# Performance work log

Measured on AMD Instinct MI355X. Metric: run time of the kernel, lower is better.

## Reference

```python
import jax, jax.numpy as jnp
import numpy as np

N_NODES = 50000
N_EDGES = 1000000
N_QUERY = 100000
NUM_FEATURES = 256
HIDDEN = 256
LABEL_DIM = 2


def glorot(key, shape):
    lim = float(np.sqrt(6.0 / (shape[0] + shape[1])))
    return jax.random.uniform(key, shape, jnp.float32, -lim, lim)


def setup_inputs() -> dict:
    key = jax.random.key(0)
    ks = jax.random.split(key, 8)
    x = jax.random.normal(ks[0], (N_NODES, NUM_FEATURES), jnp.float32)
    edge_index = jax.random.randint(ks[1], (2, N_EDGES), 0, N_NODES)
    query_edges = jax.random.randint(ks[2], (N_QUERY, 2), 0, N_NODES)
    edge_weight = jax.random.uniform(ks[3], (N_EDGES,), jnp.float32)
    W1 = glorot(ks[4], (NUM_FEATURES, HIDDEN))
    b1 = jnp.zeros((HIDDEN,), jnp.float32)
    W2 = glorot(ks[5], (HIDDEN, HIDDEN))
    b2 = jnp.zeros((HIDDEN,), jnp.float32)
    Wl = glorot(ks[6], (2 * HIDDEN, LABEL_DIM))
    bl = jnp.zeros((LABEL_DIM,), jnp.float32)
    return {"x": x, "edge_index": edge_index, "query_edges": query_edges,
            "edge_weight": edge_weight, "W1": W1, "b1": b1, "W2": W2,
            "b2": b2, "Wl": Wl, "bl": bl}


def digcn_conv(x, edge_index, edge_weight, W, b):
    # x: [N, F_in] -> h: [N, F_out]; propagate: out[dst] += w_e * h[src]
    h = x @ W
    src, dst = edge_index[0], edge_index[1]
    msg = h[src] * edge_weight[:, None]            # [E, F_out]
    agg = jax.ops.segment_sum(msg, dst, num_segments=x.shape[0])
    return agg + b


def reference(x, edge_index, query_edges, edge_weight, W1, b1, W2, b2, Wl, bl):
    h = jax.nn.relu(digcn_conv(x, edge_index, edge_weight, W1, b1))
    # dropout is identity at eval time
    h = digcn_conv(h, edge_index, edge_weight, W2, b2)
    q = jnp.concatenate((h[query_edges[:, 0]], h[query_edges[:, 1]]), axis=-1)
    logits = q @ Wl + bl
    return jax.nn.log_softmax(logits, axis=1)
```

## Files before the change

### kernel.cpp

```cpp
#include <hip/hip_runtime.h>
#include <hip/hip_bf16.h>
#include <math.h>

typedef __bf16 bf16;
typedef __bf16 v8bf __attribute__((ext_vector_type(8)));
typedef __bf16 v4bf __attribute__((ext_vector_type(4)));
typedef float  v4f  __attribute__((ext_vector_type(4)));

#define FDIM 256
#define BKT_CAP 8192
#define AROW 264
#define GEMM_BLOCKS 352
#define K3_BLOCKS 512
#define P3_BLOCKS (K3_BLOCKS - GEMM_BLOCKS)


__global__ __launch_bounds__(256) void flag_kernel(float* __restrict__ out, int n) {
  int i = blockIdx.x * 256 + threadIdx.x;
  if (i < n) out[i] = 1.0e9f;
}

__global__ __launch_bounds__(256) void k1_prep(const float* __restrict__ W1,
                                               const float* __restrict__ W2,
                                               bf16* __restrict__ Wt1,
                                               const int* __restrict__ dst,
                                               int* __restrict__ phist,
                                               const float* __restrict__ Wl,
                                               const float* __restrict__ b2,
                                               const float* __restrict__ bl,
                                               float4* __restrict__ V,
                                               float* __restrict__ cc,
                                               int E, int N, int nbkt) {
  __shared__ int h[256];
  __shared__ float sWl[1024];
  __shared__ float red[256];
  int b = blockIdx.x;
  int t = threadIdx.x;
  if (b < 256) {
    int k = b;
    Wt1[t * FDIM + k] = (bf16)W1[k * FDIM + t];
  } else if (b < 512) {
    int pb = b - 256;
    h[t] = 0;
    __syncthreads();
    for (int e = pb * 256 + t; e < E; e += 256 * 256) {
      int d = dst[e];
      d = d < 0 ? 0 : (d >= N ? N - 1 : d);
      atomicAdd(&h[d >> 8], 1);
    }
    __syncthreads();
    phist[pb * 256 + t] = h[t];
  } else {
#pragma unroll
    for (int j = 0; j < 4; ++j) sWl[j * 256 + t] = Wl[j * 256 + t];
    __syncthreads();
    const float* w2row = W2 + (size_t)t * FDIM;
    float4 acc = make_float4(0.f, 0.f, 0.f, 0.f);
    for (int j = 0; j < 256; ++j) {
      float w = w2row[j];
      acc.x += w * sWl[2 * j + 0];
      acc.y += w * sWl[2 * j + 1];
      acc.z += w * sWl[512 + 2 * j + 0];
      acc.w += w * sWl[512 + 2 * j + 1];
    }
    V[t] = acc;
    float bj = b2[t];
    red[t] = bj * (sWl[2 * t + 0] + sWl[512 + 2 * t + 0]);
    __syncthreads();
    if (t == 0) {
      float s = 0.f;
      for (int j = 0; j < 256; ++j) s += red[j];
      cc[0] = s + bl[0];
    }
    __syncthreads();
    red[t] = bj * (sWl[2 * t + 1] + sWl[512 + 2 * t + 1]);
    __syncthreads();
    if (t == 0) {
      float s = 0.f;
      for (int j = 0; j < 256; ++j) s += red[j];
      cc[1] = s + bl[1];
    }
  }
}

__global__ __launch_bounds__(256) void p2_scan(const int* __restrict__ phist,
                                               int* __restrict__ bbase,
                                               int* __restrict__ gcur,
                                               int* __restrict__ offs,
                                               int nbkt, int Nn) {
  __shared__ int wsum[4];
  int t = threadIdx.x, lane = t & 63, wv = t >> 6;
  int v = 0;
  for (int pb = 0; pb < 256; ++pb) v += phist[pb * 256 + t];
  if (t >= nbkt) v = 0;
  int x = v;
#pragma unroll
  for (int d = 1; d < 64; d <<= 1) {
    int y = __shfl_up(x, d, 64);
    if (lane >= d) x += y;
  }
  if (lane == 63) wsum[wv] = x;
  __syncthreads();
  int woff = 0;
  if (wv >= 1) woff += wsum[0];
  if (wv >= 2) woff += wsum[1];
  if (wv >= 3) woff += wsum[2];
  int incl = woff + x;
  int excl = incl - v;
  if (t < nbkt) { bbase[t] = excl; gcur[t] = excl; }
  if (t == 255) {
    bbase[nbkt] = incl;
    offs[Nn] = incl;
  }
}


__device__ inline void stage64(const float* __restrict__ A, bf16* __restrict__ As,
                               int row0, int M, int tid) {
#pragma unroll
  for (int j = 0; j < 8; ++j) {
    int g = j * 2048 + tid * 8;
    int r = g >> 8, c = g & 255;
    int gr = row0 + r; if (gr >= M) gr = M - 1;
    const float* p = A + (size_t)gr * FDIM + c;
    float4 f0 = *reinterpret_cast<const float4*>(p);
    float4 f1 = *reinterpret_cast<const float4*>(p + 4);
    v8bf o;
    o[0] = (bf16)f0.x; o[1] = (bf16)f0.y; o[2] = (bf16)f0.z; o[3] = (bf16)f0.w;
    o[4] = (bf16)f1.x; o[5] = (bf16)f1.y; o[6] = (bf16)f1.z; o[7] = (bf16)f1.w;
    *reinterpret_cast<v8bf*>(As + r * AROW + c) = o;
  }
}

__device__ inline void gemm_body(const float* __restrict__ A, const bf16* __restrict__ Bt,
                                 bf16* __restrict__ C, int M, int bid, int nblocks,
                                 bf16* __restrict__ As) {
  const int K = FDIM, N = FDIM;
  int tid = threadIdx.x;
  int wave = tid >> 6;
  int lane = tid & 63;
  int l15 = lane & 15, quad = lane >> 4;

  v8bf bfr[4][8];
#pragma unroll
  for (int nn = 0; nn < 4; ++nn) {
    const bf16* bp = Bt + (size_t)(wave * 64 + nn * 16 + l15) * K + quad * 8;
#pragma unroll
    for (int kk = 0; kk < 8; ++kk)
      bfr[nn][kk] = *reinterpret_cast<const v8bf*>(bp + kk * 32);
  }

  int ntiles = (M + 63) >> 6;
  for (int tile = bid; tile < ntiles; tile += nblocks) {
    int row0 = tile * 64;
    __syncthreads();
    stage64(A, As, row0, M, tid);
    __syncthreads();

#pragma unroll
    for (int st = 0; st < 4; ++st) {
      v8bf afr[8];
#pragma unroll
      for (int kk = 0; kk < 8; ++kk)
        afr[kk] = *reinterpret_cast<const v8bf*>(As + (st * 16 + l15) * AROW + quad * 8 + kk * 32);

      v4f acc[4];
#pragma unroll
      for (int nn = 0; nn < 4; ++nn) acc[nn] = (v4f){0.f, 0.f, 0.f, 0.f};

#pragma unroll
      for (int kk = 0; kk < 8; ++kk)
#pragma unroll
        for (int nn = 0; nn < 4; ++nn)
          acc[nn] = __builtin_amdgcn_mfma_f32_16x16x32_bf16(afr[kk], bfr[nn][kk], acc[nn], 0, 0, 0);

#pragma unroll
      for (int nn = 0; nn < 4; ++nn)
#pragma unroll
        for (int r = 0; r < 4; ++r) {
          int row = row0 + st * 16 + quad * 4 + r;
          int col = wave * 64 + nn * 16 + l15;
          if (row < M) C[(size_t)row * N + col] = (bf16)acc[nn][r];
        }
    }
  }
}

__device__ inline void p3_body(const int* __restrict__ src, const int* __restrict__ dst,
                               const float* __restrict__ ew, int* __restrict__ gcur,
                               uint2* __restrict__ tmp, int E, int N, int nbkt,
                               int pb, int nblocks, int* h, int* base, int* cnt) {
  int t = threadIdx.x;
  int chunk = (E + nblocks - 1) / nblocks;
  int lo = pb * chunk;
  int hi = lo + chunk; if (hi > E) hi = E;
  h[t] = 0; cnt[t] = 0;
  __syncthreads();
  for (int e = lo + t; e < hi; e += 256) {
    int d = dst[e];
    d = d < 0 ? 0 : (d >= N ? N - 1 : d);
    atomicAdd(&h[d >> 8], 1);
  }
  __syncthreads();
  if (t < nbkt) base[t] = atomicAdd(&gcur[t], h[t]);
  __syncthreads();
  for (int e = lo + t; e < hi; e += 256) {
    int d = dst[e];
    d = d < 0 ? 0 : (d >= N ? N - 1 : d);
    int b = d >> 8;
    int sv = src[e];
    sv = sv < 0 ? 0 : (sv >= N ? N - 1 : sv);
    unsigned int u = __float_as_uint(ew[e]);
    unsigned int wbits = ((u + 0x7FFFu + ((u >> 16) & 1u)) & 0xFFFF0000u);
    unsigned int meta = wbits | (unsigned int)(sv & 0xFFFF);
    int r = atomicAdd(&cnt[b], 1);
    int pos = base[b] + r;
    if (pos >= 0 && pos < E) tmp[pos] = make_uint2(meta, (unsigned int)d);
  }
}

__global__ __launch_bounds__(256, 2) void k3_gemm1_p3(const float* __restrict__ x,
                                                      const bf16* __restrict__ Wt1,
                                                      bf16* __restrict__ bufT, int M,
                                                      const int* __restrict__ src,
                                                      const int* __restrict__ dst,
                                                      const float* __restrict__ ew,
                                                      int* __restrict__ gcur,
                                                      uint2* __restrict__ tmp,
                                                      int E, int N, int nbkt) {
  __shared__ bf16 As[64 * AROW];
  __shared__ int h[256], base[256], cnt[256];
  if (blockIdx.x < GEMM_BLOCKS)
    gemm_body(x, Wt1, bufT, M, blockIdx.x, GEMM_BLOCKS, As);
  else
    p3_body(src, dst, ew, gcur, tmp, E, N, nbkt, blockIdx.x - GEMM_BLOCKS, P3_BLOCKS,
            h, base, cnt);
}

__global__ __launch_bounds__(256) void p4_sort(const uint2* __restrict__ tmp,
                                               const int* __restrict__ bbase,
                                               unsigned int* __restrict__ pmeta,
                                               int* __restrict__ offs,
                                               int Nn, int E) {
  __shared__ uint2 ent[BKT_CAP];
  __shared__ int h2[256], ex2[256], c2[256];
  __shared__ int wsum[4];
  int b = blockIdx.x, t = threadIdx.x, lane = t & 63, wv = t >> 6;
  int s0 = bbase[b], s1 = bbase[b + 1];
  int count = s1 - s0;
  if (count < 0) count = 0;
  if (count > BKT_CAP) count = BKT_CAP;
  for (int i = t; i < count; i += 256) ent[i] = tmp[s0 + i];
  h2[t] = 0; c2[t] = 0;
  __syncthreads();
  for (int i = t; i < count; i += 256) atomicAdd(&h2[ent[i].y & 255u], 1);
  __syncthreads();
  int v = h2[t];
  int x = v;
#pragma unroll
  for (int d = 1; d < 64; d <<= 1) {
    int y = __shfl_up(x, d, 64);
    if (lane >= d) x += y;
  }
  if (lane == 63) wsum[wv] = x;
  __syncthreads();
  int woff = 0;
  if (wv >= 1) woff += wsum[0];
  if (wv >= 2) woff += wsum[1];
  if (wv >= 3) woff += wsum[2];
  int excl = woff + x - v;
  ex2[t] = excl;
  int node = (b << 8) + t;
  if (node < Nn) offs[node] = s0 + excl;
  __syncthreads();
  for (int i = t; i < count; i += 256) {
    int l = (int)(ent[i].y & 255u);
    int r = atomicAdd(&c2[l], 1);
    int pos = s0 + ex2[l] + r;
    if (pos >= 0 && pos < E) pmeta[pos] = ent[i].x;
  }
}

__global__ __launch_bounds__(256) void agg1G(const bf16* __restrict__ T,
                                             const unsigned int* __restrict__ pmeta,
                                             const int* __restrict__ offsets,
                                             const float* __restrict__ bias,
                                             const float4* __restrict__ V,
                                             float4* __restrict__ G, int N, int E) {
  int wid = blockIdx.x * 4 + (threadIdx.x >> 6);
  int nw = gridDim.x * 4;
  int lane = threadIdx.x & 63;
  int f = lane * 4;
  const bf16* Tf = T + f;

  float4 bb = *reinterpret_cast<const float4*>(bias + f);
  float4 v0 = V[f + 0], v1 = V[f + 1], v2 = V[f + 2], v3 = V[f + 3];

  for (int node = wid; node < N; node += nw) {
    int nb = __builtin_amdgcn_readfirstlane(node);
    int beg = offsets[nb], end = offsets[nb + 1];
    beg = beg < 0 ? 0 : (beg > E ? E : beg);
    end = end < beg ? beg : (end > E ? E : end);
    int cnt = end - beg;
    const unsigned int* m = pmeta + beg;

    float a0 = 0.f, a1 = 0.f, a2 = 0.f, a3 = 0.f;
    int p = 0;
    for (; p + 8 <= cnt; p += 8) {
      unsigned int mv0 = m[p + 0], mv1 = m[p + 1], mv2 = m[p + 2], mv3 = m[p + 3];
      unsigned int mv4 = m[p + 4], mv5 = m[p + 5], mv6 = m[p + 6], mv7 = m[p + 7];
      v4bf t0 = *reinterpret_cast<const v4bf*>(Tf + ((size_t)(mv0 & 0xFFFFu) << 8));
      v4bf t1 = *reinterpret_cast<const v4bf*>(Tf + ((size_t)(mv1 & 0xFFFFu) << 8));
      v4bf t2 = *reinterpret_cast<const v4bf*>(Tf + ((size_t)(mv2 & 0xFFFFu) << 8));
      v4bf t3 = *reinterpret_cast<const v4bf*>(Tf + ((size_t)(mv3 & 0xFFFFu) << 8));
      v4bf t4 = *reinterpret_cast<const v4bf*>(Tf + ((size_t)(mv4 & 0xFFFFu) << 8));
      v4bf t5 = *reinterpret_cast<const v4bf*>(Tf + ((size_t)(mv5 & 0xFFFFu) << 8));
      v4bf t6 = *reinterpret_cast<const v4bf*>(Tf + ((size_t)(mv6 & 0xFFFFu) << 8));
      v4bf t7 = *reinterpret_cast<const v4bf*>(Tf + ((size_t)(mv7 & 0xFFFFu) << 8));
      float w0 = __uint_as_float(mv0 & 0xFFFF0000u);
      float w1 = __uint_as_float(mv1 & 0xFFFF0000u);
      float w2 = __uint_as_float(mv2 & 0xFFFF0000u);
      float w3 = __uint_as_float(mv3 & 0xFFFF0000u);
      float w4 = __uint_as_float(mv4 & 0xFFFF0000u);
      float w5 = __uint_as_float(mv5 & 0xFFFF0000u);
      float w6 = __uint_as_float(mv6 & 0xFFFF0000u);
      float w7 = __uint_as_float(mv7 & 0xFFFF0000u);
      a0 += w0 * (float)t0[0]; a1 += w0 * (float)t0[1]; a2 += w0 * (float)t0[2]; a3 += w0 * (float)t0[3];
      a0 += w1 * (float)t1[0]; a1 += w1 * (float)t1[1]; a2 += w1 * (float)t1[2]; a3 += w1 * (float)t1[3];
      a0 += w2 * (float)t2[0]; a1 += w2 * (float)t2[1]; a2 += w2 * (float)t2[2]; a3 += w2 * (float)t2[3];
      a0 += w3 * (float)t3[0]; a1 += w3 * (float)t3[1]; a2 += w3 * (float)t3[2]; a3 += w3 * (float)t3[3];
      a0 += w4 * (float)t4[0]; a1 += w4 * (float)t4[1]; a2 += w4 * (float)t4[2]; a3 += w4 * (float)t4[3];
      a0 += w5 * (float)t5[0]; a1 += w5 * (float)t5[1]; a2 += w5 * (float)t5[2]; a3 += w5 * (float)t5[3];
      a0 += w6 * (float)t6[0]; a1 += w6 * (float)t6[1]; a2 += w6 * (float)t6[2]; a3 += w6 * (float)t6[3];
      a0 += w7 * (float)t7[0]; a1 += w7 * (float)t7[1]; a2 += w7 * (float)t7[2]; a3 += w7 * (float)t7[3];
    }
    for (; p < cnt; ++p) {
      unsigned int mv = m[p];
      float w = __uint_as_float(mv & 0xFFFF0000u);
      v4bf tv = *reinterpret_cast<const v4bf*>(Tf + ((size_t)(mv & 0xFFFFu) << 8));
      a0 += w * (float)tv[0];
      a1 += w * (float)tv[1];
      a2 += w * (float)tv[2];
      a3 += w * (float)tv[3];
    }

    float r0 = fmaxf(a0 + bb.x, 0.f);
    float r1 = fmaxf(a1 + bb.y, 0.f);
    float r2 = fmaxf(a2 + bb.z, 0.f);
    float r3 = fmaxf(a3 + bb.w, 0.f);

    float gx = r0 * v0.x + r1 * v1.x + r2 * v2.x + r3 * v3.x;
    float gy = r0 * v0.y + r1 * v1.y + r2 * v2.y + r3 * v3.y;
    float gz = r0 * v0.z + r1 * v1.z + r2 * v2.z + r3 * v3.z;
    float gw = r0 * v0.w + r1 * v1.w + r2 * v2.w + r3 * v3.w;
#pragma unroll
    for (int d = 32; d > 0; d >>= 1) {
      gx += __shfl_down(gx, d, 64);
      gy += __shfl_down(gy, d, 64);
      gz += __shfl_down(gz, d, 64);
      gw += __shfl_down(gw, d, 64);
    }
    if (lane == 0) G[node] = make_float4(gx, gy, gz, gw);
  }
}

__global__ __launch_bounds__(256) void aggP(const float4* __restrict__ G,
                                            const unsigned int* __restrict__ pmeta,
                                            const int* __restrict__ offsets,
                                            float4* __restrict__ P, int N, int E) {
  int node = blockIdx.x * 256 + threadIdx.x;
  if (node >= N) return;
  int beg = offsets[node], end = offsets[node + 1];
  beg = beg < 0 ? 0 : (beg > E ? E : beg);
  end = end < beg ? beg : (end > E ? E : end);
  float ax = 0.f, ay = 0.f, az = 0.f, aw = 0.f;
  int p = beg;
  for (; p + 4 <= end; p += 4) {
    unsigned int m0 = pmeta[p + 0], m1 = pmeta[p + 1], m2 = pmeta[p + 2], m3 = pmeta[p + 3];
    int s0 = (int)(m0 & 0xFFFFu); s0 = s0 >= N ? N - 1 : s0;
    int s1 = (int)(m1 & 0xFFFFu); s1 = s1 >= N ? N - 1 : s1;
    int s2 = (int)(m2 & 0xFFFFu); s2 = s2 >= N ? N - 1 : s2;
    int s3 = (int)(m3 & 0xFFFFu); s3 = s3 >= N ? N - 1 : s3;
    float4 g0 = G[s0], g1 = G[s1], g2 = G[s2], g3 = G[s3];
    float w0 = __uint_as_float(m0 & 0xFFFF0000u);
    float w1 = __uint_as_float(m1 & 0xFFFF0000u);
    float w2 = __uint_as_float(m2 & 0xFFFF0000u);
    float w3 = __uint_as_float(m3 & 0xFFFF0000u);
    ax += w0 * g0.x + w1 * g1.x + w2 * g2.x + w3 * g3.x;
    ay += w0 * g0.y + w1 * g1.y + w2 * g2.y + w3 * g3.y;
    az += w0 * g0.z + w1 * g1.z + w2 * g2.z + w3 * g3.z;
    aw += w0 * g0.w + w1 * g1.w + w2 * g2.w + w3 * g3.w;
  }
  for (; p < end; ++p) {
    unsigned int mm = pmeta[p];
    int s = (int)(mm & 0xFFFFu); s = s >= N ? N - 1 : s;
    float w = __uint_as_float(mm & 0xFFFF0000u);
    float4 g = G[s];
    ax += w * g.x; ay += w * g.y; az += w * g.z; aw += w * g.w;
  }
  P[node] = make_float4(ax, ay, az, aw);
}

__global__ __launch_bounds__(256) void query_small(const int* __restrict__ qe,
                                                   const float4* __restrict__ P,
                                                   const float* __restrict__ cc,
                                                   float* __restrict__ out, int Q, int N) {
  int q = blockIdx.x * 256 + threadIdx.x;
  if (q >= Q) return;
  int n0 = qe[2 * q + 0]; n0 = n0 < 0 ? 0 : (n0 >= N ? N - 1 : n0);
  int n1 = qe[2 * q + 1]; n1 = n1 < 0 ? 0 : (n1 >= N ? N - 1 : n1);
  float4 p0 = P[n0];
  float4 p1 = P[n1];
  float l0 = p0.x + p1.z + cc[0];
  float l1 = p0.y + p1.w + cc[1];
  float m = fmaxf(l0, l1);
  float lse = m + logf(expf(l0 - m) + expf(l1 - m));
  out[2 * q + 0] = l0 - lse;
  out[2 * q + 1] = l1 - lse;
}


extern "C" void kernel_launch(void* const* d_in, const int* in_sizes, int n_in,
                              void* d_out, int out_size, void* d_ws, size_t ws_size,
                              hipStream_t stream) {
  const float* x  = (const float*)d_in[0];
  const int*   ei = (const int*)d_in[1];
  const int*   qe = (const int*)d_in[2];
  const float* ew = (const float*)d_in[3];
  const float* W1 = (const float*)d_in[4];
  const float* b1 = (const float*)d_in[5];
  const float* W2 = (const float*)d_in[6];
  const float* b2 = (const float*)d_in[7];
  const float* Wl = (const float*)d_in[8];
  const float* bl = (const float*)d_in[9];

  int N = in_sizes[0] / FDIM;
  int E = in_sizes[1] / 2;
  int Q = in_sizes[2] / 2;
  const int* srcv = ei;
  const int* dstv = ei + E;
  int nbkt = (N + 255) >> 8;

  size_t off = 0;
  auto alloc = [&](size_t bytes) -> void* {
    void* p = (char*)d_ws + off;
    off += (bytes + 255) & ~(size_t)255;
    return p;
  };
  bf16* bufT  = (bf16*)alloc((size_t)N * FDIM * 2);
  uint2* tmp  = (uint2*)alloc((size_t)E * 8);
  bf16* Wt1   = (bf16*)alloc((size_t)FDIM * FDIM * 2);
  int* offs   = (int*)alloc((size_t)(N + 1) * 4);
  unsigned int* pmeta = (unsigned int*)alloc((size_t)E * 4);
  float4* G   = (float4*)alloc((size_t)N * 16);
  float4* P   = (float4*)alloc((size_t)N * 16);
  float4* V   = (float4*)alloc(256 * 16);
  float* cc   = (float*)alloc(2 * 4);
  int* phist  = (int*)alloc(256 * 256 * 4);
  int* bbase  = (int*)alloc(257 * 4);
  int* gcur   = (int*)alloc(256 * 4);

  if (off > ws_size) {
    flag_kernel<<<(out_size + 255) / 256, 256, 0, stream>>>((float*)d_out, out_size);
    return;
  }

  k1_prep<<<513, 256, 0, stream>>>(W1, W2, Wt1, dstv, phist, Wl, b2, bl, V, cc,
                                   E, N, nbkt);
  p2_scan<<<1, 256, 0, stream>>>(phist, bbase, gcur, offs, nbkt, N);
  k3_gemm1_p3<<<K3_BLOCKS, 256, 0, stream>>>(x, Wt1, bufT, N,
                                             srcv, dstv, ew, gcur, tmp, E, N, nbkt);
  p4_sort<<<nbkt, 256, 0, stream>>>(tmp, bbase, pmeta, offs, N, E);

  agg1G<<<2048, 256, 0, stream>>>(bufT, pmeta, offs, b1, V, G, N, E);

  aggP<<<(N + 255) / 256, 256, 0, stream>>>(G, pmeta, offs, P, N, E);

  query_small<<<(Q + 255) / 256, 256, 0, stream>>>(qe, P, cc, (float*)d_out, Q, N);
}
```

Before: 249.4 us.

## Precompute per-block scatter bases, split fused GEMM/scatter, stage sort output, split aggP per node

The scan kernel now builds per-partition, per-bucket base offsets from the chunked histogram, so the scatter kernel no longer recounts edges or uses global atomics. The fused GEMM+scatter kernel is split into two separate kernels, and the GEMM grid now has one block per tile. p4_sort stages its sorted output in LDS and writes it out contiguously. aggP uses four lanes per node and reduces them with shuffles. This trades an extra kernel launch and a larger scan for less redundant histogram work, coalesced writes and more parallelism in aggP. The GEMM and scatter no longer overlap.

Result: no change. 252.1 us (+1.1%).

```diff
diff --git a/kernel.cpp b/kernel.cpp
--- a/kernel.cpp
+++ b/kernel.cpp
@@ -10,9 +10,6 @@
 #define FDIM 256
 #define BKT_CAP 8192
 #define AROW 264
-#define GEMM_BLOCKS 352
-#define K3_BLOCKS 512
-#define P3_BLOCKS (K3_BLOCKS - GEMM_BLOCKS)
 
 
 __global__ __launch_bounds__(256) void flag_kernel(float* __restrict__ out, int n) {
@@ -41,9 +38,12 @@
     Wt1[t * FDIM + k] = (bf16)W1[k * FDIM + t];
   } else if (b < 512) {
     int pb = b - 256;
+    int chunk = (E + 255) >> 8;
+    int lo = pb * chunk;
+    int hi = lo + chunk; if (hi > E) hi = E;
     h[t] = 0;
     __syncthreads();
-    for (int e = pb * 256 + t; e < E; e += 256 * 256) {
+    for (int e = lo + t; e < hi; e += 256) {
       int d = dst[e];
       d = d < 0 ? 0 : (d >= N ? N - 1 : d);
       atomicAdd(&h[d >> 8], 1);
@@ -85,7 +85,7 @@
 
 __global__ __launch_bounds__(256) void p2_scan(const int* __restrict__ phist,
                                                int* __restrict__ bbase,
-                                               int* __restrict__ gcur,
+                                               int* __restrict__ pbase,
                                                int* __restrict__ offs,
                                                int nbkt, int Nn) {
   __shared__ int wsum[4];
@@ -107,13 +107,17 @@
   if (wv >= 3) woff += wsum[2];
   int incl = woff + x;
   int excl = incl - v;
-  if (t < nbkt) { bbase[t] = excl; gcur[t] = excl; }
+  if (t < nbkt) bbase[t] = excl;
   if (t == 255) {
     bbase[nbkt] = incl;
     offs[Nn] = incl;
   }
-}
-
+  int run = excl;
+  for (int pb = 0; pb < 256; ++pb) {
+    pbase[pb * 256 + t] = run;
+    run += phist[pb * 256 + t];
+  }
+}
 
 __device__ inline void stage64(const float* __restrict__ A, bf16* __restrict__ As,
                                int row0, int M, int tid) {
@@ -132,9 +136,10 @@
   }
 }
 
-__device__ inline void gemm_body(const float* __restrict__ A, const bf16* __restrict__ Bt,
-                                 bf16* __restrict__ C, int M, int bid, int nblocks,
-                                 bf16* __restrict__ As) {
+__global__ __launch_bounds__(256, 2) void gemm1(const float* __restrict__ A,
+                                                const bf16* __restrict__ Bt,
+                                                bf16* __restrict__ C, int M) {
+  __shared__ bf16 As[64 * AROW];
   const int K = FDIM, N = FDIM;
   int tid = threadIdx.x;
   int wave = tid >> 6;
@@ -151,7 +156,7 @@
   }
 
   int ntiles = (M + 63) >> 6;
-  for (int tile = bid; tile < ntiles; tile += nblocks) {
+  for (int tile = blockIdx.x; tile < ntiles; tile += gridDim.x) {
     int row0 = tile * 64;
     __syncthreads();
     stage64(A, As, row0, M, tid);
@@ -186,23 +191,20 @@
   }
 }
 
-__device__ inline void p3_body(const int* __restrict__ src, const int* __restrict__ dst,
-                               const float* __restrict__ ew, int* __restrict__ gcur,
-                               uint2* __restrict__ tmp, int E, int N, int nbkt,
-                               int pb, int nblocks, int* h, int* base, int* cnt) {
-  int t = threadIdx.x;
-  int chunk = (E + nblocks - 1) / nblocks;
+__global__ __launch_bounds__(256) void p3_scatter(const int* __restrict__ src,
+                                                  const int* __restrict__ dst,
+                                                  const float* __restrict__ ew,
+                                                  const int* __restrict__ pbase,
+                                                  uint2* __restrict__ tmp,
+                                                  int E, int N) {
+  __shared__ int cnt[256];
+  __shared__ int base_s[256];
+  int pb = blockIdx.x, t = threadIdx.x;
+  int chunk = (E + 255) >> 8;
   int lo = pb * chunk;
   int hi = lo + chunk; if (hi > E) hi = E;
-  h[t] = 0; cnt[t] = 0;
-  __syncthreads();
-  for (int e = lo + t; e < hi; e += 256) {
-    int d = dst[e];
-    d = d < 0 ? 0 : (d >= N ? N - 1 : d);
-    atomicAdd(&h[d >> 8], 1);
-  }
-  __syncthreads();
-  if (t < nbkt) base[t] = atomicAdd(&gcur[t], h[t]);
+  cnt[t] = 0;
+  base_s[t] = pbase[pb * 256 + t];
   __syncthreads();
   for (int e = lo + t; e < hi; e += 256) {
     int d = dst[e];
@@ -214,35 +216,18 @@
     unsigned int wbits = ((u + 0x7FFFu + ((u >> 16) & 1u)) & 0xFFFF0000u);
     unsigned int meta = wbits | (unsigned int)(sv & 0xFFFF);
     int r = atomicAdd(&cnt[b], 1);
-    int pos = base[b] + r;
+    int pos = base_s[b] + r;
     if (pos >= 0 && pos < E) tmp[pos] = make_uint2(meta, (unsigned int)d);
   }
 }
 
-__global__ __launch_bounds__(256, 2) void k3_gemm1_p3(const float* __restrict__ x,
-                                                      const bf16* __restrict__ Wt1,
-                                                      bf16* __restrict__ bufT, int M,
-                                                      const int* __restrict__ src,
-                                                      const int* __restrict__ dst,
-                                                      const float* __restrict__ ew,
-                                                      int* __restrict__ gcur,
-                                                      uint2* __restrict__ tmp,
-                                                      int E, int N, int nbkt) {
-  __shared__ bf16 As[64 * AROW];
-  __shared__ int h[256], base[256], cnt[256];
-  if (blockIdx.x < GEMM_BLOCKS)
-    gemm_body(x, Wt1, bufT, M, blockIdx.x, GEMM_BLOCKS, As);
-  else
-    p3_body(src, dst, ew, gcur, tmp, E, N, nbkt, blockIdx.x - GEMM_BLOCKS, P3_BLOCKS,
-            h, base, cnt);
-}
-
-__global__ __launch_bounds__(256) void p4_sort(const uint2* __restrict__ tmp,
-                                               const int* __restrict__ bbase,
-                                               unsigned int* __restrict__ pmeta,
-                                               int* __restrict__ offs,
-                                               int Nn, int E) {
+__global__ __launch_bounds__(256, 1) void p4_sort(const uint2* __restrict__ tmp,
+                                                  const int* __restrict__ bbase,
+                                                  unsigned int* __restrict__ pmeta,
+                                                  int* __restrict__ offs,
+                                                  int Nn, int E) {
   __shared__ uint2 ent[BKT_CAP];
+  __shared__ unsigned int outm[BKT_CAP];
   __shared__ int h2[256], ex2[256], c2[256];
   __shared__ int wsum[4];
   int b = blockIdx.x, t = threadIdx.x, lane = t & 63, wv = t >> 6;
@@ -276,9 +261,10 @@
   for (int i = t; i < count; i += 256) {
     int l = (int)(ent[i].y & 255u);
     int r = atomicAdd(&c2[l], 1);
-    int pos = s0 + ex2[l] + r;
-    if (pos >= 0 && pos < E) pmeta[pos] = ent[i].x;
-  }
+    outm[ex2[l] + r] = ent[i].x;
+  }
+  __syncthreads();
+  for (int i = t; i < count; i += 256) pmeta[s0 + i] = outm[i];
 }
 
 __global__ __launch_bounds__(256) void agg1G(const bf16* __restrict__ T,
@@ -368,37 +354,38 @@
                                             const unsigned int* __restrict__ pmeta,
                                             const int* __restrict__ offsets,
                                             float4* __restrict__ P, int N, int E) {
-  int node = blockIdx.x * 256 + threadIdx.x;
+  int node = blockIdx.x * 64 + (threadIdx.x >> 2);
   if (node >= N) return;
+  int j = threadIdx.x & 3;
   int beg = offsets[node], end = offsets[node + 1];
   beg = beg < 0 ? 0 : (beg > E ? E : beg);
   end = end < beg ? beg : (end > E ? E : end);
   float ax = 0.f, ay = 0.f, az = 0.f, aw = 0.f;
-  int p = beg;
-  for (; p + 4 <= end; p += 4) {
-    unsigned int m0 = pmeta[p + 0], m1 = pmeta[p + 1], m2 = pmeta[p + 2], m3 = pmeta[p + 3];
+  int p = beg + j;
+  for (; p + 4 < end; p += 8) {
+    unsigned int m0 = pmeta[p], m1 = pmeta[p + 4];
     int s0 = (int)(m0 & 0xFFFFu); s0 = s0 >= N ? N - 1 : s0;
     int s1 = (int)(m1 & 0xFFFFu); s1 = s1 >= N ? N - 1 : s1;
-    int s2 = (int)(m2 & 0xFFFFu); s2 = s2 >= N ? N - 1 : s2;
-    int s3 = (int)(m3 & 0xFFFFu); s3 = s3 >= N ? N - 1 : s3;
-    float4 g0 = G[s0], g1 = G[s1], g2 = G[s2], g3 = G[s3];
+    float4 g0 = G[s0], g1 = G[s1];
     float w0 = __uint_as_float(m0 & 0xFFFF0000u);
     float w1 = __uint_as_float(m1 & 0xFFFF0000u);
-    float w2 = __uint_as_float(m2 & 0xFFFF0000u);
-    float w3 = __uint_as_float(m3 & 0xFFFF0000u);
-    ax += w0 * g0.x + w1 * g1.x + w2 * g2.x + w3 * g3.x;
-    ay += w0 * g0.y + w1 * g1.y + w2 * g2.y + w3 * g3.y;
-    az += w0 * g0.z + w1 * g1.z + w2 * g2.z + w3 * g3.z;
-    aw += w0 * g0.w + w1 * g1.w + w2 * g2.w + w3 * g3.w;
-  }
-  for (; p < end; ++p) {
+    ax += w0 * g0.x + w1 * g1.x;
+    ay += w0 * g0.y + w1 * g1.y;
+    az += w0 * g0.z + w1 * g1.z;
+    aw += w0 * g0.w + w1 * g1.w;
+  }
+  if (p < end) {
     unsigned int mm = pmeta[p];
     int s = (int)(mm & 0xFFFFu); s = s >= N ? N - 1 : s;
     float w = __uint_as_float(mm & 0xFFFF0000u);
     float4 g = G[s];
     ax += w * g.x; ay += w * g.y; az += w * g.z; aw += w * g.w;
   }
-  P[node] = make_float4(ax, ay, az, aw);
+  ax += __shfl_xor(ax, 1, 64); ax += __shfl_xor(ax, 2, 64);
+  ay += __shfl_xor(ay, 1, 64); ay += __shfl_xor(ay, 2, 64);
+  az += __shfl_xor(az, 1, 64); az += __shfl_xor(az, 2, 64);
+  aw += __shfl_xor(aw, 1, 64); aw += __shfl_xor(aw, 2, 64);
+  if (j == 0) P[node] = make_float4(ax, ay, az, aw);
 }
 
 __global__ __launch_bounds__(256) void query_small(const int* __restrict__ qe,
@@ -440,6 +427,7 @@
   const int* srcv = ei;
   const int* dstv = ei + E;
   int nbkt = (N + 255) >> 8;
+  int ntiles = (N + 63) >> 6;
 
   size_t off = 0;
   auto alloc = [&](size_t bytes) -> void* {
@@ -457,8 +445,8 @@
   float4* V   = (float4*)alloc(256 * 16);
   float* cc   = (float*)alloc(2 * 4);
   int* phist  = (int*)alloc(256 * 256 * 4);
+  int* pbase  = (int*)alloc(256 * 256 * 4);
   int* bbase  = (int*)alloc(257 * 4);
-  int* gcur   = (int*)alloc(256 * 4);
 
   if (off > ws_size) {
     flag_kernel<<<(out_size + 255) / 256, 256, 0, stream>>>((float*)d_out, out_size);
@@ -467,14 +455,14 @@
 
   k1_prep<<<513, 256, 0, stream>>>(W1, W2, Wt1, dstv, phist, Wl, b2, bl, V, cc,
                                    E, N, nbkt);
-  p2_scan<<<1, 256, 0, stream>>>(phist, bbase, gcur, offs, nbkt, N);
-  k3_gemm1_p3<<<K3_BLOCKS, 256, 0, stream>>>(x, Wt1, bufT, N,
-                                             srcv, dstv, ew, gcur, tmp, E, N, nbkt);
+  p2_scan<<<1, 256, 0, stream>>>(phist, bbase, pbase, offs, nbkt, N);
+  gemm1<<<ntiles, 256, 0, stream>>>(x, Wt1, bufT, N);
+  p3_scatter<<<256, 256, 0, stream>>>(srcv, dstv, ew, pbase, tmp, E, N);
   p4_sort<<<nbkt, 256, 0, stream>>>(tmp, bbase, pmeta, offs, N, E);
 
   agg1G<<<2048, 256, 0, stream>>>(bufT, pmeta, offs, b1, V, G, N, E);
 
-  aggP<<<(N + 255) / 256, 256, 0, stream>>>(G, pmeta, offs, P, N, E);
+  aggP<<<(N * 4 + 255) / 256, 256, 0, stream>>>(G, pmeta, offs, P, N, E);
 
   query_small<<<(Q + 255) / 256, 256, 0, stream>>>(qe, P, cc, (float*)d_out, Q, N);
 }
```
